# Kernel optimization log

Hardware: AMD Instinct MI355X
Metric: run time of the kernel (lower is better)

Reference implementation:

```python
import jax, jax.numpy as jnp
import numpy as np

B, N, DIM, H, DH, M = 4, 1024, 1024, 16, 64, 16  # batch, seq, model dim, heads, head dim, num_mem_kv
QK_SCALE = 10.0  # qk_norm_scale


def l2norm(t, eps=1e-12):
    # F.normalize(t, dim=-1) with clamp_min(eps), groups=1
    n = jnp.linalg.norm(t, axis=-1, keepdims=True)
    return t / jnp.maximum(n, eps)


def rotate_half(x):
    # interleaved pairs: (x0,x1) -> (-x1, x0)
    x = x.reshape(*x.shape[:-1], -1, 2)
    x1, x2 = x[..., 0], x[..., 1]
    return jnp.stack((-x2, x1), axis=-1).reshape(*x.shape[:-2], x.shape[-2] * 2)


def apply_rope(t, freqs):
    # freqs: [n, d], t: [b, h, n, d]
    return t * jnp.cos(freqs) + rotate_half(t) * jnp.sin(freqs)


def setup_inputs() -> dict:
    key = jax.random.key(0)
    ks = jax.random.split(key, 14)
    x = jax.random.normal(ks[0], (B, N, DIM), dtype=jnp.float32)
    # rotary freqs: outer(pos, inv_freq) with each freq repeated twice (interleaved pairs)
    pos = jnp.arange(N, dtype=jnp.float32)
    inv_freq = 1.0 / (10000.0 ** (jnp.arange(0, DH, 2, dtype=jnp.float32) / DH))
    freqs = jnp.repeat(pos[:, None] * inv_freq[None, :], 2, axis=-1)  # [N, DH]
    s = 0.02
    Wq = jax.random.normal(ks[1], (DIM, H * DH), dtype=jnp.float32) * s
    Wk = jax.random.normal(ks[2], (DIM, H * DH), dtype=jnp.float32) * s
    Wv = jax.random.normal(ks[3], (DIM, H * DH), dtype=jnp.float32) * s
    q_scale = 1.0 + 0.1 * jax.random.normal(ks[4], (H, 1, DH), dtype=jnp.float32)
    k_scale = 1.0 + 0.1 * jax.random.normal(ks[5], (H, 1, DH), dtype=jnp.float32)
    mem_k = jax.random.normal(ks[6], (H, M, DH), dtype=jnp.float32)
    mem_v = jax.random.normal(ks[7], (H, M, DH), dtype=jnp.float32)
    W_pre = jnp.eye(H, dtype=jnp.float32) + 0.05 * jax.random.normal(ks[8], (H, H), dtype=jnp.float32)
    W_post = jnp.eye(H, dtype=jnp.float32) + 0.05 * jax.random.normal(ks[9], (H, H), dtype=jnp.float32)
    W_hgate = jax.random.normal(ks[10], (DIM, H), dtype=jnp.float32) * s
    b_hgate = jnp.full((H,), 2.0, dtype=jnp.float32)
    W_vgate = jax.random.normal(ks[11], (DIM, H * DH), dtype=jnp.float32) * s
    b_vgate = jnp.full((H * DH,), 2.0, dtype=jnp.float32)
    Wo = jax.random.normal(ks[12], (H * DH, DIM), dtype=jnp.float32) * s
    return dict(x=x, freqs=freqs, Wq=Wq, Wk=Wk, Wv=Wv, q_scale=q_scale, k_scale=k_scale,
                mem_k=mem_k, mem_v=mem_v, W_pre=W_pre, W_post=W_post,
                W_hgate=W_hgate, b_hgate=b_hgate, W_vgate=W_vgate, b_vgate=b_vgate, Wo=Wo)


def reference(x, freqs, Wq, Wk, Wv, q_scale, k_scale, mem_k, mem_v,
              W_pre, W_post, W_hgate, b_hgate, W_vgate, b_vgate, Wo):
    b, n, _ = x.shape
    # projections -> [b, h, n, dh]
    q = (x @ Wq).reshape(b, n, H, DH).transpose(0, 2, 1, 3)
    k = (x @ Wk).reshape(b, n, H, DH).transpose(0, 2, 1, 3)
    v = (x @ Wv).reshape(b, n, H, DH).transpose(0, 2, 1, 3)
    # qk l2-norm (groups=1) + learned per-head dim scales
    q = l2norm(q) * q_scale
    k = l2norm(k) * k_scale
    # rotary (xpos_scale = None -> scale 1)
    q = apply_rope(q, freqs)
    k = apply_rope(k, freqs)
    # memory key/values, prepended along the kv sequence axis
    mk = (l2norm(mem_k) * k_scale)[None].repeat(b, axis=0)  # [b,h,M,dh]
    mv = mem_v[None].repeat(b, axis=0)
    k = jnp.concatenate((mk, k), axis=-2)  # [b,h,M+n,dh]
    v = jnp.concatenate((mv, v), axis=-2)
    i, j = q.shape[-2], k.shape[-2]
    dots = jnp.einsum('bhid,bhjd->bhij', q, k) * QK_SCALE
    dots = jnp.einsum('bhij,gh->bgij', dots, W_pre)  # pre-softmax talking heads
    # causal mask (memory slots at the front are always visible)
    qpos = jnp.arange(i)
    kpos = jnp.arange(j)
    causal = kpos[None, :] > (qpos[:, None] + (j - i))  # True -> masked
    mask_value = -jnp.finfo(dots.dtype).max
    dots = jnp.where(causal[None, None], mask_value, dots)
    attn = jax.nn.softmax(dots, axis=-1)
    attn = jnp.einsum('bhij,gh->bgij', attn, W_post)  # post-softmax talking heads
    out = jnp.einsum('bhij,bhjd->bhid', attn, v)  # [b,h,n,dh]
    # per-head value gate
    head_gate = jax.nn.sigmoid(x @ W_hgate + b_hgate)  # [b,n,h]
    out = out * head_gate.transpose(0, 2, 1)[..., None]
    out = out.transpose(0, 2, 1, 3).reshape(b, n, H * DH)
    # per-dim value gate (sigmoid)
    out = out * jax.nn.sigmoid(x @ W_vgate + b_vgate)
    return out @ Wo
```

## Files before the change

### kernel.cpp

```cpp
#include <hip/hip_runtime.h>
#include <hip/hip_bf16.h>
#include <cmath>

typedef __attribute__((ext_vector_type(8))) short short8;
typedef __attribute__((ext_vector_type(4))) float f32x4;

__device__ __forceinline__ unsigned short to_bf(float f) {
  __hip_bfloat16 h = __float2bfloat16(f);
  return __builtin_bit_cast(unsigned short, h);
}

#define SWZS(ir) ((((ir) & 1) << 4) | (((ir) & 6) << 1))

__global__ __launch_bounds__(256)
void cvt_bf16x4(const float* __restrict__ in, unsigned short* __restrict__ out, int n4)
{
  int i = blockIdx.x * 256 + threadIdx.x;
  if (i < n4) {
    float4 v = ((const float4*)in)[i];
    ushort4 o;
    o.x = to_bf(v.x); o.y = to_bf(v.y); o.z = to_bf(v.z); o.w = to_bf(v.w);
    ((ushort4*)out)[i] = o;
  }
}

__global__ __launch_bounds__(256)
void transpose_to_bf(const float* __restrict__ W, unsigned short* __restrict__ WT)
{
  __shared__ float tile[64][65];
  const int n0 = blockIdx.x * 64, k0 = blockIdx.y * 64;
  const int t = threadIdx.x, c = t & 63, r4 = t >> 6;
#pragma unroll
  for (int q = 0; q < 16; ++q) {
    int r = (q << 2) + r4;
    tile[r][c] = W[(size_t)(k0 + r) * 1024 + n0 + c];
  }
  __syncthreads();
#pragma unroll
  for (int q = 0; q < 16; ++q) {
    int r = (q << 2) + r4;
    WT[(size_t)(n0 + r) * 1024 + k0 + c] = to_bf(tile[c][r]);
  }
}

__global__ __launch_bounds__(256)
void transpose4_to_bf(const float* __restrict__ W0, const float* __restrict__ W1,
                      const float* __restrict__ W2, const float* __restrict__ W3,
                      unsigned short* __restrict__ WT4)
{
  __shared__ float tile[64][65];
  const float* W = (blockIdx.z == 0) ? W0 : (blockIdx.z == 1) ? W1
                 : (blockIdx.z == 2) ? W2 : W3;
  const int n0 = blockIdx.x * 64, k0 = blockIdx.y * 64;
  const int t = threadIdx.x, c = t & 63, r4 = t >> 6;
#pragma unroll
  for (int q = 0; q < 16; ++q) {
    int r = (q << 2) + r4;
    tile[r][c] = W[(size_t)(k0 + r) * 1024 + n0 + c];
  }
  __syncthreads();
  const size_t zoff = (size_t)blockIdx.z << 10;
#pragma unroll
  for (int q = 0; q < 16; ++q) {
    int r = (q << 2) + r4;
    WT4[(zoff + n0 + r) * 1024 + k0 + c] = to_bf(tile[c][r]);
  }
}

__global__ __launch_bounds__(256)
void gemm_bf128(const unsigned short* __restrict__ A, const unsigned short* __restrict__ BT,
                float* __restrict__ C)
{
  __shared__ __align__(16) unsigned short Ab[128 * 36];
  __shared__ __align__(16) unsigned short Bb[64 * 36];
  const int t = threadIdx.x, lane = t & 63, w = t >> 6;
  const int m = lane & 15, quad = lane >> 4;
  const int row0 = blockIdx.y << 7, col0 = blockIdx.x << 6;

  const int r0 = t >> 2, kp0 = t & 3;
  const int r1 = 64 + r0;

  f32x4 acc[2][4];
#pragma unroll
  for (int mi = 0; mi < 2; ++mi)
#pragma unroll
    for (int ni = 0; ni < 4; ++ni) acc[mi][ni] = (f32x4){0.f, 0.f, 0.f, 0.f};

  uint4 pa0 = *(const uint4*)(A + (size_t)(row0 + r0) * 1024 + kp0 * 8);
  uint4 pa1 = *(const uint4*)(A + (size_t)(row0 + r1) * 1024 + kp0 * 8);
  uint4 pb0 = *(const uint4*)(BT + (size_t)(col0 + r0) * 1024 + kp0 * 8);

  for (int kk = 0; kk < 1024; kk += 32) {
    *(uint4*)((char*)Ab + r0 * 72 + kp0 * 16) = pa0;
    *(uint4*)((char*)Ab + r1 * 72 + kp0 * 16) = pa1;
    *(uint4*)((char*)Bb + r0 * 72 + kp0 * 16) = pb0;
    __syncthreads();
    if (kk + 32 < 1024) {
      pa0 = *(const uint4*)(A + (size_t)(row0 + r0) * 1024 + kk + 32 + kp0 * 8);
      pa1 = *(const uint4*)(A + (size_t)(row0 + r1) * 1024 + kk + 32 + kp0 * 8);
      pb0 = *(const uint4*)(BT + (size_t)(col0 + r0) * 1024 + kk + 32 + kp0 * 8);
    }
    short8 af[2], bf[4];
#pragma unroll
    for (int mi = 0; mi < 2; ++mi)
      af[mi] = *(const short8*)((char*)Ab + ((w << 5) + (mi << 4) + m) * 72 + quad * 16);
#pragma unroll
    for (int ni = 0; ni < 4; ++ni)
      bf[ni] = *(const short8*)((char*)Bb + ((ni << 4) + m) * 72 + quad * 16);
#pragma unroll
    for (int mi = 0; mi < 2; ++mi)
#pragma unroll
      for (int ni = 0; ni < 4; ++ni)
        acc[mi][ni] = __builtin_amdgcn_mfma_f32_16x16x32_bf16(af[mi], bf[ni], acc[mi][ni], 0, 0, 0);
    __syncthreads();
  }
#pragma unroll
  for (int mi = 0; mi < 2; ++mi)
#pragma unroll
    for (int ni = 0; ni < 4; ++ni)
#pragma unroll
      for (int reg = 0; reg < 4; ++reg) {
        int mrow = row0 + (w << 5) + (mi << 4) + (quad << 2) + reg;
        int ncol = col0 + (ni << 4) + m;
        C[((size_t)mrow << 10) + ncol] = acc[mi][ni][reg];
      }
}

__global__ __launch_bounds__(256)
void gemm_qkvg(const unsigned short* __restrict__ A, const unsigned short* __restrict__ BT4,
               float* __restrict__ q_lin, float* __restrict__ k_lin,
               unsigned short* __restrict__ vallT, float* __restrict__ vgbuf,
               const float* __restrict__ b_vg)
{
  __shared__ __align__(16) unsigned short Ab[128 * 36];
  __shared__ __align__(16) unsigned short Bb[64 * 36];
  const int t = threadIdx.x, lane = t & 63, w = t >> 6;
  const int m = lane & 15, quad = lane >> 4;
  const int row0 = blockIdx.y << 7, col0 = blockIdx.x << 6;
  const int sector = col0 >> 10;

  const int r0 = t >> 2, kp0 = t & 3;
  const int r1 = 64 + r0;

  f32x4 acc[2][4];
#pragma unroll
  for (int mi = 0; mi < 2; ++mi)
#pragma unroll
    for (int ni = 0; ni < 4; ++ni) acc[mi][ni] = (f32x4){0.f, 0.f, 0.f, 0.f};

  uint4 pa0 = *(const uint4*)(A + (size_t)(row0 + r0) * 1024 + kp0 * 8);
  uint4 pa1 = *(const uint4*)(A + (size_t)(row0 + r1) * 1024 + kp0 * 8);
  uint4 pb0 = *(const uint4*)(BT4 + (size_t)(col0 + r0) * 1024 + kp0 * 8);

  for (int kk = 0; kk < 1024; kk += 32) {
    *(uint4*)((char*)Ab + r0 * 72 + kp0 * 16) = pa0;
    *(uint4*)((char*)Ab + r1 * 72 + kp0 * 16) = pa1;
    *(uint4*)((char*)Bb + r0 * 72 + kp0 * 16) = pb0;
    __syncthreads();
    if (kk + 32 < 1024) {
      pa0 = *(const uint4*)(A + (size_t)(row0 + r0) * 1024 + kk + 32 + kp0 * 8);
      pa1 = *(const uint4*)(A + (size_t)(row0 + r1) * 1024 + kk + 32 + kp0 * 8);
      pb0 = *(const uint4*)(BT4 + (size_t)(col0 + r0) * 1024 + kk + 32 + kp0 * 8);
    }
    short8 af[2], bf[4];
#pragma unroll
    for (int mi = 0; mi < 2; ++mi)
      af[mi] = *(const short8*)((char*)Ab + ((w << 5) + (mi << 4) + m) * 72 + quad * 16);
#pragma unroll
    for (int ni = 0; ni < 4; ++ni)
      bf[ni] = *(const short8*)((char*)Bb + ((ni << 4) + m) * 72 + quad * 16);
#pragma unroll
    for (int mi = 0; mi < 2; ++mi)
#pragma unroll
      for (int ni = 0; ni < 4; ++ni)
        acc[mi][ni] = __builtin_amdgcn_mfma_f32_16x16x32_bf16(af[mi], bf[ni], acc[mi][ni], 0, 0, 0);
    __syncthreads();
  }
#pragma unroll
  for (int mi = 0; mi < 2; ++mi)
#pragma unroll
    for (int ni = 0; ni < 4; ++ni)
#pragma unroll
      for (int reg = 0; reg < 4; ++reg) {
        int mrow = row0 + (w << 5) + (mi << 4) + (quad << 2) + reg;
        int nl = (col0 & 1023) + (ni << 4) + m;
        float v = acc[mi][ni][reg];
        if (sector == 0) {
          q_lin[((size_t)mrow << 10) + nl] = v;
        } else if (sector == 1) {
          k_lin[((size_t)mrow << 10) + nl] = v;
        } else if (sector == 2) {
          int bb = mrow >> 10, nn = mrow & 1023;
          vallT[((size_t)((bb << 10) + nl)) * 1056 + 16 + nn] = to_bf(v);
        } else {
          float s = v + b_vg[nl];
          vgbuf[((size_t)mrow << 10) + nl] = 1.f / (1.f + __expf(-s));
        }
      }
}

__global__ __launch_bounds__(256)
void hgate_proj(const float* __restrict__ x, const float* __restrict__ W,
                const float* __restrict__ bias, float* __restrict__ hg)
{
  int G = blockIdx.x * 256 + threadIdx.x;
  int row = G >> 4, h = G & 15;
  const float4* x4 = (const float4*)(x + ((size_t)row << 10));
  float acc = 0.f;
#pragma unroll 4
  for (int k4 = 0; k4 < 256; ++k4) {
    float4 xv = x4[k4];
    int kb = k4 << 2;
    acc += xv.x * W[(kb + 0) * 16 + h] + xv.y * W[(kb + 1) * 16 + h]
         + xv.z * W[(kb + 2) * 16 + h] + xv.w * W[(kb + 3) * 16 + h];
  }
  float v = acc + bias[h];
  hg[(row << 4) + h] = 1.f / (1.f + __expf(-v));
}

__global__ __launch_bounds__(256)
void q_post_bf(const float* __restrict__ q_lin, const float* __restrict__ scale,
               const float* __restrict__ freqs, unsigned short* __restrict__ qb)
{
  int gid = blockIdx.x * 256 + threadIdx.x;
  int d = gid & 63;
  int row = gid >> 6;
  int h = row & 15;
  int n = (row >> 4) & 1023;
  float v = q_lin[gid];
  float ss = v * v;
#pragma unroll
  for (int off = 32; off; off >>= 1) ss += __shfl_xor(ss, off);
  v = v / fmaxf(sqrtf(ss), 1e-12f) * scale[(h << 6) + d];
  float f = freqs[(n << 6) + d];
  float other = __shfl_xor(v, 1);
  float rot = (d & 1) ? other : -other;
  qb[gid] = to_bf((v * cosf(f) + rot * sinf(f)) * 10.f);
}

__global__ __launch_bounds__(256)
void k_post_bf(const float* __restrict__ k_lin, const float* __restrict__ scale,
               const float* __restrict__ freqs, unsigned short* __restrict__ kall)
{
  int gid = blockIdx.x * 256 + threadIdx.x;
  int d = gid & 63;
  int row = gid >> 6;
  int h = row & 15;
  int n = (row >> 4) & 1023;
  int b = row >> 14;
  float v = k_lin[gid];
  float ss = v * v;
#pragma unroll
  for (int off = 32; off; off >>= 1) ss += __shfl_xor(ss, off);
  v = v / fmaxf(sqrtf(ss), 1e-12f) * scale[(h << 6) + d];
  float f = freqs[(n << 6) + d];
  float other = __shfl_xor(v, 1);
  float rot = (d & 1) ? other : -other;
  float out = v * cosf(f) + rot * sinf(f);
  kall[(size_t)(b * 1056 + 16 + n) * 1024 + (h << 6) + d] = to_bf(out);
}

__global__ __launch_bounds__(256)
void mem_build(const float* __restrict__ mem_k, const float* __restrict__ mem_v,
               const float* __restrict__ k_scale,
               unsigned short* __restrict__ kall, unsigned short* __restrict__ vallT)
{
  int gid = blockIdx.x * 256 + threadIdx.x;
  int d = gid & 63;
  int row = gid >> 6;
  int h = row >> 4, mm = row & 15;
  float v = mem_k[gid];
  float ss = v * v;
#pragma unroll
  for (int off = 32; off; off >>= 1) ss += __shfl_xor(ss, off);
  unsigned short kb = to_bf(v / fmaxf(sqrtf(ss), 1e-12f) * k_scale[(h << 6) + d]);
  unsigned short vb = to_bf(mem_v[gid]);
#pragma unroll
  for (int b = 0; b < 4; ++b) {
    kall[(size_t)(b * 1056 + mm) * 1024 + (h << 6) + d] = kb;
    vallT[(size_t)((b << 10) + (h << 6) + d) * 1056 + mm] = vb;
  }
}


__global__ __launch_bounds__(256)
void attn_lsum(const unsigned short* __restrict__ qb, const unsigned short* __restrict__ kall,
               const float* __restrict__ W_pre, float* __restrict__ Lbuf)
{
  __shared__ float sS[16 * 16 * 32];
  __shared__ f32x4 sWpre4[64];

  const int t = threadIdx.x, lane = t & 63, w = t >> 6;
  const int m = lane & 15, quad = lane >> 4;
  if (t < 64) {
    int h = t >> 2, p4 = t & 3;
    sWpre4[t] = (f32x4){W_pre[(4 * p4 + 0) * 16 + h], W_pre[(4 * p4 + 1) * 16 + h],
                        W_pre[(4 * p4 + 2) * 16 + h], W_pre[(4 * p4 + 3) * 16 + h]};
  }

  const int blk = blockIdx.x;
  const int u0 = (4352 * blk) / 768, u1 = (4352 * (blk + 1)) / 768;
  if (u0 == u1) return;

  int accu = 0, bi = 0;
  while (true) {
    int un = (((bi & 63) + 1) >> 1) + 1;
    if (accu + un > u0) break;
    accu += un; ++bi;
  }
  int b = bi >> 6, it = bi & 63, uoff = u0 - accu;

  short8 afr[4][2];
  float partL[16];
  bool fresh = true;

  for (int u = u0; u < u1; ++u) {
    const int i0 = it << 4;
    if (fresh) {
#pragma unroll
      for (int hh = 0; hh < 4; ++hh)
#pragma unroll
        for (int kk = 0; kk < 2; ++kk)
          afr[hh][kk] = *(const short8*)(qb + (((size_t)(b << 10) + i0 + m) << 10)
                                         + ((w << 2) + hh) * 64 + kk * 32 + quad * 8);
#pragma unroll
      for (int g = 0; g < 16; ++g) partL[g] = 0.f;
      fresh = false;
    }
    const int j0 = uoff << 5;
#pragma unroll
    for (int sub = 0; sub < 2; ++sub) {
      const int js = j0 + (sub << 4);
#pragma unroll
      for (int hh = 0; hh < 4; ++hh) {
        f32x4 s = (f32x4){0.f, 0.f, 0.f, 0.f};
#pragma unroll
        for (int kk = 0; kk < 2; ++kk) {
          short8 bfr = *(const short8*)(kall + ((size_t)(b * 1056 + js + m) << 10)
                                        + ((w << 2) + hh) * 64 + kk * 32 + quad * 8);
          s = __builtin_amdgcn_mfma_f32_16x16x32_bf16(afr[hh][kk], bfr, s, 0, 0, 0);
        }
#pragma unroll
        for (int reg = 0; reg < 4; ++reg) {
          int irow = (quad << 2) + reg;
          sS[(((w << 2) + hh) * 16 + irow) * 32 + (((sub << 4) + m) ^ SWZS(irow))] = s[reg];
        }
      }
    }
    __syncthreads();
    {
      const int i_l = t >> 4, j_l = t & 15;
      const int ig = i0 + i_l;
      const int vs = SWZS(i_l);
      const int sc0 = j_l ^ vs, sc1 = (16 + j_l) ^ vs;
      float ch0[16], ch1[16];
#pragma unroll
      for (int h = 0; h < 16; ++h) {
        ch0[h] = sS[(h * 16 + i_l) * 32 + sc0];
        ch1[h] = sS[(h * 16 + i_l) * 32 + sc1];
      }
      f32x4 a0[4], a1[4];
#pragma unroll
      for (int p = 0; p < 4; ++p) { a0[p] = (f32x4){0.f,0.f,0.f,0.f}; a1[p] = a0[p]; }
#pragma unroll
      for (int h = 0; h < 16; ++h) {
        float c0 = ch0[h], c1 = ch1[h];
#pragma unroll
        for (int p = 0; p < 4; ++p) {
          f32x4 wv = sWpre4[(h << 2) + p];
          a0[p] += wv * c0;
          a1[p] += wv * c1;
        }
      }
      const bool ok0 = (j0 + j_l) <= ig + 16;
      const bool ok1 = (j0 + 16 + j_l) <= ig + 16;
#pragma unroll
      for (int p = 0; p < 4; ++p)
#pragma unroll
        for (int e = 0; e < 4; ++e) {
          float v0 = ok0 ? __expf(a0[p][e] - 20.f) : 0.f;
          float v1 = ok1 ? __expf(a1[p][e] - 20.f) : 0.f;
          partL[(p << 2) + e] += v0 + v1;
        }
    }
    __syncthreads();
    ++uoff;
    if (uoff == ((it + 1) >> 1) + 1) {
#pragma unroll
      for (int g = 0; g < 16; ++g) {
        float v = partL[g];
        v += __shfl_xor(v, 1); v += __shfl_xor(v, 2);
        v += __shfl_xor(v, 4); v += __shfl_xor(v, 8);
        if (m == 0)
          atomicAdd(&Lbuf[(((size_t)(b << 10) + i0 + (w << 2) + quad) << 4) + g], v);
      }
      ++bi; b = bi >> 6; it = bi & 63; uoff = 0; fresh = true;
    }
  }
  if (!fresh) {
    const int i0 = it << 4;
#pragma unroll
    for (int g = 0; g < 16; ++g) {
      float v = partL[g];
      v += __shfl_xor(v, 1); v += __shfl_xor(v, 2);
      v += __shfl_xor(v, 4); v += __shfl_xor(v, 8);
      if (m == 0)
        atomicAdd(&Lbuf[(((size_t)(b << 10) + i0 + (w << 2) + quad) << 4) + g], v);
    }
  }
}

__global__ __launch_bounds__(256)
void attn_pv2(const unsigned short* __restrict__ qb, const unsigned short* __restrict__ kall,
              const unsigned short* __restrict__ vallT, const float* __restrict__ W_pre,
              const float* __restrict__ W_post, const float* __restrict__ Lbuf,
              float* __restrict__ Obuf)
{
  __shared__ float sS[16 * 16 * 32];
  __shared__ __align__(16) unsigned short sE[16 * 16 * 32];
  __shared__ f32x4 sWpre4[64], sWpost4[64];
  __shared__ float sIL[256];

  const int t = threadIdx.x, lane = t & 63, w = t >> 6;
  const int m = lane & 15, quad = lane >> 4;
  if (t < 64) {
    int h = t >> 2, p4 = t & 3;
    sWpre4[t]  = (f32x4){W_pre[(4 * p4 + 0) * 16 + h],  W_pre[(4 * p4 + 1) * 16 + h],
                         W_pre[(4 * p4 + 2) * 16 + h],  W_pre[(4 * p4 + 3) * 16 + h]};
    sWpost4[t] = (f32x4){W_post[(4 * p4 + 0) * 16 + h], W_post[(4 * p4 + 1) * 16 + h],
                         W_post[(4 * p4 + 2) * 16 + h], W_post[(4 * p4 + 3) * 16 + h]};
  }

  const int blk = blockIdx.x;
  const int u0 = (4352 * blk) / 768, u1 = (4352 * (blk + 1)) / 768;
  if (u0 == u1) return;

  int accu = 0, bi = 0;
  while (true) {
    int un = (((bi & 63) + 1) >> 1) + 1;
    if (accu + un > u0) break;
    accu += un; ++bi;
  }
  int b = bi >> 6, it = bi & 63, uoff = u0 - accu;

  short8 afr[4][2];
  f32x4 oacc[4][4];
  bool fresh = true;

  for (int u = u0; u < u1; ++u) {
    const int i0 = it << 4;
    if (fresh) {
#pragma unroll
      for (int hh = 0; hh < 4; ++hh)
#pragma unroll
        for (int kk = 0; kk < 2; ++kk)
          afr[hh][kk] = *(const short8*)(qb + (((size_t)(b << 10) + i0 + m) << 10)
                                         + ((w << 2) + hh) * 64 + kk * 32 + quad * 8);
#pragma unroll
      for (int a = 0; a < 4; ++a)
#pragma unroll
        for (int dt = 0; dt < 4; ++dt) oacc[a][dt] = (f32x4){0.f, 0.f, 0.f, 0.f};
      sIL[t] = 1.f / Lbuf[(((size_t)(b << 10) + i0 + (t >> 4)) << 4) + (t & 15)];
      fresh = false;
    }
    const int j0 = uoff << 5;
#pragma unroll
    for (int sub = 0; sub < 2; ++sub) {
      const int js = j0 + (sub << 4);
#pragma unroll
      for (int hh = 0; hh < 4; ++hh) {
        f32x4 s = (f32x4){0.f, 0.f, 0.f, 0.f};
#pragma unroll
        for (int kk = 0; kk < 2; ++kk) {
          short8 bfr = *(const short8*)(kall + ((size_t)(b * 1056 + js + m) << 10)
                                        + ((w << 2) + hh) * 64 + kk * 32 + quad * 8);
          s = __builtin_amdgcn_mfma_f32_16x16x32_bf16(afr[hh][kk], bfr, s, 0, 0, 0);
        }
#pragma unroll
        for (int reg = 0; reg < 4; ++reg) {
          int irow = (quad << 2) + reg;
          sS[(((w << 2) + hh) * 16 + irow) * 32 + (((sub << 4) + m) ^ SWZS(irow))] = s[reg];
        }
      }
    }
    __syncthreads();
    {
      const int i_l = t >> 4, j_l = t & 15;
      const int ig = i0 + i_l;
      const int vs = SWZS(i_l);
      const int sc0 = j_l ^ vs, sc1 = (16 + j_l) ^ vs;
      const int r3s = i_l & 3;
      const int eo0 = ((((j_l >> 3) ^ r3s) << 3) | (j_l & 7));
      const int eo1 = ((((2 + (j_l >> 3)) ^ r3s) << 3) | (j_l & 7));
      float ch0[16], ch1[16];
#pragma unroll
      for (int h = 0; h < 16; ++h) {
        ch0[h] = sS[(h * 16 + i_l) * 32 + sc0];
        ch1[h] = sS[(h * 16 + i_l) * 32 + sc1];
      }
      f32x4 a0[4], a1[4];
#pragma unroll
      for (int p = 0; p < 4; ++p) { a0[p] = (f32x4){0.f,0.f,0.f,0.f}; a1[p] = a0[p]; }
#pragma unroll
      for (int h = 0; h < 16; ++h) {
        float c0 = ch0[h], c1 = ch1[h];
#pragma unroll
        for (int p = 0; p < 4; ++p) {
          f32x4 wv = sWpre4[(h << 2) + p];
          a0[p] += wv * c0;
          a1[p] += wv * c1;
        }
      }
      const bool ok0 = (j0 + j_l) <= ig + 16;
      const bool ok1 = (j0 + 16 + j_l) <= ig + 16;
      float e0[16], e1[16];
#pragma unroll
      for (int p = 0; p < 4; ++p)
#pragma unroll
        for (int e = 0; e < 4; ++e) {
          int g = (p << 2) + e;
          float il = sIL[(i_l << 4) + g];
          e0[g] = ok0 ? __expf(a0[p][e] - 20.f) * il : 0.f;
          e1[g] = ok1 ? __expf(a1[p][e] - 20.f) * il : 0.f;
        }
      f32x4 b0[4], b1[4];
#pragma unroll
      for (int p = 0; p < 4; ++p) { b0[p] = (f32x4){0.f,0.f,0.f,0.f}; b1[p] = b0[p]; }
#pragma unroll
      for (int g = 0; g < 16; ++g) {
        float c0 = e0[g], c1 = e1[g];
#pragma unroll
        for (int p = 0; p < 4; ++p) {
          f32x4 wv = sWpost4[(g << 2) + p];
          b0[p] += wv * c0;
          b1[p] += wv * c1;
        }
      }
#pragma unroll
      for (int p = 0; p < 4; ++p)
#pragma unroll
        for (int e = 0; e < 4; ++e) {
          int g2 = (p << 2) + e;
          sE[(g2 * 16 + i_l) * 32 + eo0] = to_bf(b0[p][e]);
          sE[(g2 * 16 + i_l) * 32 + eo1] = to_bf(b1[p][e]);
        }
    }
    __syncthreads();
#pragma unroll
    for (int gl = 0; gl < 4; ++gl) {
      const int g2 = (w << 2) + gl;
      short8 a = *(const short8*)(sE + (g2 * 16 + m) * 32 + ((quad ^ (m & 3)) << 3));
#pragma unroll
      for (int dt = 0; dt < 4; ++dt) {
        short8 bv = *(const short8*)(vallT + ((size_t)((b << 10) + g2 * 64 + dt * 16 + m)) * 1056
                                     + j0 + quad * 8);
        oacc[gl][dt] = __builtin_amdgcn_mfma_f32_16x16x32_bf16(a, bv, oacc[gl][dt], 0, 0, 0);
      }
    }
    ++uoff;
    if (uoff == ((it + 1) >> 1) + 1) {
#pragma unroll
      for (int gl = 0; gl < 4; ++gl) {
        int g2 = (w << 2) + gl;
#pragma unroll
        for (int dt = 0; dt < 4; ++dt)
#pragma unroll
          for (int reg = 0; reg < 4; ++reg)
            atomicAdd(&Obuf[(((size_t)(b << 10) + i0 + (quad << 2) + reg) << 10)
                            + g2 * 64 + dt * 16 + m], oacc[gl][dt][reg]);
      }
      ++bi; b = bi >> 6; it = bi & 63; uoff = 0; fresh = true;
    }
  }
  if (!fresh) {
    const int i0 = it << 4;
#pragma unroll
    for (int gl = 0; gl < 4; ++gl) {
      int g2 = (w << 2) + gl;
#pragma unroll
      for (int dt = 0; dt < 4; ++dt)
#pragma unroll
        for (int reg = 0; reg < 4; ++reg)
          atomicAdd(&Obuf[(((size_t)(b << 10) + i0 + (quad << 2) + reg) << 10)
                          + g2 * 64 + dt * 16 + m], oacc[gl][dt][reg]);
    }
  }
}

__global__ __launch_bounds__(256)
void gate_out(const float* __restrict__ Obuf, const float* __restrict__ hgate,
              const float* __restrict__ vgate, unsigned short* __restrict__ aob)
{
  int i4 = blockIdx.x * 256 + threadIdx.x;
  float4 o = ((const float4*)Obuf)[i4];
  int base = i4 << 2;
  int row = base >> 10, hd = base & 1023, h = hd >> 6;
  float hg = hgate[(row << 4) + h];
  float4 vg = ((const float4*)vgate)[i4];
  ushort4 r;
  r.x = to_bf(o.x * hg * vg.x);
  r.y = to_bf(o.y * hg * vg.y);
  r.z = to_bf(o.z * hg * vg.z);
  r.w = to_bf(o.w * hg * vg.w);
  ((ushort4*)aob)[i4] = r;
}

extern "C" void kernel_launch(void* const* d_in, const int* in_sizes, int n_in,
                              void* d_out, int out_size, void* d_ws, size_t ws_size,
                              hipStream_t stream)
{
  const float* x       = (const float*)d_in[0];
  const float* freqs   = (const float*)d_in[1];
  const float* Wq      = (const float*)d_in[2];
  const float* Wk      = (const float*)d_in[3];
  const float* Wv      = (const float*)d_in[4];
  const float* q_scale = (const float*)d_in[5];
  const float* k_scale = (const float*)d_in[6];
  const float* mem_k   = (const float*)d_in[7];
  const float* mem_v   = (const float*)d_in[8];
  const float* W_pre   = (const float*)d_in[9];
  const float* W_post  = (const float*)d_in[10];
  const float* W_hg    = (const float*)d_in[11];
  const float* b_hg    = (const float*)d_in[12];
  const float* W_vg    = (const float*)d_in[13];
  const float* b_vg    = (const float*)d_in[14];
  const float* Wo      = (const float*)d_in[15];
  float* out = (float*)d_out;
  float* ws  = (float*)d_ws;

  float* q_lin = ws;
  unsigned short* aob = (unsigned short*)ws;
  float* Lbuf  = ws + 4128768;
  float* k_lin = ws + 4194304;
  float* Obuf  = k_lin;
  float* vgbuf = ws + 8388608;
  float* hgbuf = ws + 12582912;
  unsigned short* xb   = (unsigned short*)(ws + 12713984);
  unsigned short* qb   = xb;
  unsigned short* kall = (unsigned short*)(ws + 14811136);
  unsigned short* vallT= (unsigned short*)(ws + 16973824);
  unsigned short* wb4  = kall;

  dim3 blk(256);
  cvt_bf16x4<<<4096, blk, 0, stream>>>(x, xb, 1048576);
  hgate_proj<<<256, blk, 0, stream>>>(x, W_hg, b_hg, hgbuf);
  transpose4_to_bf<<<dim3(16, 16, 4), blk, 0, stream>>>(Wq, Wk, Wv, W_vg, wb4);
  gemm_qkvg<<<dim3(64, 32), blk, 0, stream>>>(xb, wb4, q_lin, k_lin, vallT, vgbuf, b_vg);
  q_post_bf<<<16384, blk, 0, stream>>>(q_lin, q_scale, freqs, qb);
  k_post_bf<<<16384, blk, 0, stream>>>(k_lin, k_scale, freqs, kall);
  mem_build<<<64, blk, 0, stream>>>(mem_k, mem_v, k_scale, kall, vallT);
  hipMemsetAsync(Lbuf, 0, (65536 + 4194304) * sizeof(float), stream);
  attn_lsum<<<768, blk, 0, stream>>>(qb, kall, W_pre, Lbuf);
  attn_pv2<<<768, blk, 0, stream>>>(qb, kall, vallT, W_pre, W_post, Lbuf, Obuf);
  gate_out<<<4096, blk, 0, stream>>>(Obuf, hgbuf, vgbuf, aob);
  transpose_to_bf<<<dim3(16, 16), blk, 0, stream>>>(Wo, wb4);
  gemm_bf128<<<dim3(16, 32), blk, 0, stream>>>(aob, wb4, out);
}
```

Baseline: 507.6 us.

## Use direct global-to-LDS loads with double-buffered tiles in projection GEMMs

Both bf16 GEMM kernels now stage A and B tiles straight from global memory into LDS with global_load_lds instead of going through registers, and alternate between two LDS buffers so the next tile loads while the current one feeds MFMA. This is meant to hide load latency and remove register staging and one barrier per iteration. The padded 72-byte row stride becomes an unpadded 64-byte stride, which may add LDS bank conflicts on the fragment reads. It also relies on the implicit per-wave contiguous LDS layout matching the row/k mapping.

```diff
diff --git a/kernel.cpp b/kernel.cpp
--- a/kernel.cpp
+++ b/kernel.cpp
@@ -8,6 +8,11 @@
 __device__ __forceinline__ unsigned short to_bf(float f) {
   __hip_bfloat16 h = __float2bfloat16(f);
   return __builtin_bit_cast(unsigned short, h);
+}
+
+__device__ __forceinline__ void gload_lds16(const void* g, void* l) {
+  __builtin_amdgcn_global_load_lds((const __attribute__((address_space(1))) void*)g,
+                                   (__attribute__((address_space(3))) void*)l, 16, 0, 0);
 }
 
 #define SWZS(ir) ((((ir) & 1) << 4) | (((ir) & 6) << 1))
@@ -71,14 +76,13 @@
 void gemm_bf128(const unsigned short* __restrict__ A, const unsigned short* __restrict__ BT,
                 float* __restrict__ C)
 {
-  __shared__ __align__(16) unsigned short Ab[128 * 36];
-  __shared__ __align__(16) unsigned short Bb[64 * 36];
+  __shared__ __align__(16) unsigned short Ab[2][128 * 32];
+  __shared__ __align__(16) unsigned short Bb[2][64 * 32];
   const int t = threadIdx.x, lane = t & 63, w = t >> 6;
   const int m = lane & 15, quad = lane >> 4;
   const int row0 = blockIdx.y << 7, col0 = blockIdx.x << 6;
 
   const int r0 = t >> 2, kp0 = t & 3;
-  const int r1 = 64 + r0;
 
   f32x4 acc[2][4];
 #pragma unroll
@@ -86,33 +90,36 @@
 #pragma unroll
     for (int ni = 0; ni < 4; ++ni) acc[mi][ni] = (f32x4){0.f, 0.f, 0.f, 0.f};
 
-  uint4 pa0 = *(const uint4*)(A + (size_t)(row0 + r0) * 1024 + kp0 * 8);
-  uint4 pa1 = *(const uint4*)(A + (size_t)(row0 + r1) * 1024 + kp0 * 8);
-  uint4 pb0 = *(const uint4*)(BT + (size_t)(col0 + r0) * 1024 + kp0 * 8);
-
+  const unsigned short* gA0 = A + (size_t)(row0 + r0) * 1024 + kp0 * 8;
+  const unsigned short* gA1 = A + (size_t)(row0 + 64 + r0) * 1024 + kp0 * 8;
+  const unsigned short* gB0 = BT + (size_t)(col0 + r0) * 1024 + kp0 * 8;
+  const int wb = w << 10;
+
+#define STAGE_WO(buf, kk) do {                                            \
+    gload_lds16(gA0 + (kk), (char*)&Ab[buf][0] + wb);                     \
+    gload_lds16(gA1 + (kk), (char*)&Ab[buf][0] + 4096 + wb);              \
+    gload_lds16(gB0 + (kk), (char*)&Bb[buf][0] + wb);                     \
+  } while (0)
+
+  STAGE_WO(0, 0);
+  __syncthreads();
+  int cur = 0;
   for (int kk = 0; kk < 1024; kk += 32) {
-    *(uint4*)((char*)Ab + r0 * 72 + kp0 * 16) = pa0;
-    *(uint4*)((char*)Ab + r1 * 72 + kp0 * 16) = pa1;
-    *(uint4*)((char*)Bb + r0 * 72 + kp0 * 16) = pb0;
-    __syncthreads();
-    if (kk + 32 < 1024) {
-      pa0 = *(const uint4*)(A + (size_t)(row0 + r0) * 1024 + kk + 32 + kp0 * 8);
-      pa1 = *(const uint4*)(A + (size_t)(row0 + r1) * 1024 + kk + 32 + kp0 * 8);
-      pb0 = *(const uint4*)(BT + (size_t)(col0 + r0) * 1024 + kk + 32 + kp0 * 8);
-    }
+    if (kk + 32 < 1024) STAGE_WO(cur ^ 1, kk + 32);
     short8 af[2], bf[4];
 #pragma unroll
     for (int mi = 0; mi < 2; ++mi)
-      af[mi] = *(const short8*)((char*)Ab + ((w << 5) + (mi << 4) + m) * 72 + quad * 16);
+      af[mi] = *(const short8*)((char*)&Ab[cur][0] + ((w << 5) + (mi << 4) + m) * 64 + quad * 16);
 #pragma unroll
     for (int ni = 0; ni < 4; ++ni)
-      bf[ni] = *(const short8*)((char*)Bb + ((ni << 4) + m) * 72 + quad * 16);
+      bf[ni] = *(const short8*)((char*)&Bb[cur][0] + ((ni << 4) + m) * 64 + quad * 16);
 #pragma unroll
     for (int mi = 0; mi < 2; ++mi)
 #pragma unroll
       for (int ni = 0; ni < 4; ++ni)
         acc[mi][ni] = __builtin_amdgcn_mfma_f32_16x16x32_bf16(af[mi], bf[ni], acc[mi][ni], 0, 0, 0);
     __syncthreads();
+    cur ^= 1;
   }
 #pragma unroll
   for (int mi = 0; mi < 2; ++mi)
@@ -132,15 +139,14 @@
                unsigned short* __restrict__ vallT, float* __restrict__ vgbuf,
                const float* __restrict__ b_vg)
 {
-  __shared__ __align__(16) unsigned short Ab[128 * 36];
-  __shared__ __align__(16) unsigned short Bb[64 * 36];
+  __shared__ __align__(16) unsigned short Ab[2][128 * 32];
+  __shared__ __align__(16) unsigned short Bb[2][64 * 32];
   const int t = threadIdx.x, lane = t & 63, w = t >> 6;
   const int m = lane & 15, quad = lane >> 4;
   const int row0 = blockIdx.y << 7, col0 = blockIdx.x << 6;
   const int sector = col0 >> 10;
 
   const int r0 = t >> 2, kp0 = t & 3;
-  const int r1 = 64 + r0;
 
   f32x4 acc[2][4];
 #pragma unroll
@@ -148,33 +154,36 @@
 #pragma unroll
     for (int ni = 0; ni < 4; ++ni) acc[mi][ni] = (f32x4){0.f, 0.f, 0.f, 0.f};
 
-  uint4 pa0 = *(const uint4*)(A + (size_t)(row0 + r0) * 1024 + kp0 * 8);
-  uint4 pa1 = *(const uint4*)(A + (size_t)(row0 + r1) * 1024 + kp0 * 8);
-  uint4 pb0 = *(const uint4*)(BT4 + (size_t)(col0 + r0) * 1024 + kp0 * 8);
-
+  const unsigned short* gA0 = A + (size_t)(row0 + r0) * 1024 + kp0 * 8;
+  const unsigned short* gA1 = A + (size_t)(row0 + 64 + r0) * 1024 + kp0 * 8;
+  const unsigned short* gB0 = BT4 + (size_t)(col0 + r0) * 1024 + kp0 * 8;
+  const int wb = w << 10;
+
+#define STAGE_QK(buf, kk) do {                                            \
+    gload_lds16(gA0 + (kk), (char*)&Ab[buf][0] + wb);                     \
+    gload_lds16(gA1 + (kk), (char*)&Ab[buf][0] + 4096 + wb);              \
+    gload_lds16(gB0 + (kk), (char*)&Bb[buf][0] + wb);                     \
+  } while (0)
+
+  STAGE_QK(0, 0);
+  __syncthreads();
+  int cur = 0;
   for (int kk = 0; kk < 1024; kk += 32) {
-    *(uint4*)((char*)Ab + r0 * 72 + kp0 * 16) = pa0;
-    *(uint4*)((char*)Ab + r1 * 72 + kp0 * 16) = pa1;
-    *(uint4*)((char*)Bb + r0 * 72 + kp0 * 16) = pb0;
-    __syncthreads();
-    if (kk + 32 < 1024) {
-      pa0 = *(const uint4*)(A + (size_t)(row0 + r0) * 1024 + kk + 32 + kp0 * 8);
-      pa1 = *(const uint4*)(A + (size_t)(row0 + r1) * 1024 + kk + 32 + kp0 * 8);
-      pb0 = *(const uint4*)(BT4 + (size_t)(col0 + r0) * 1024 + kk + 32 + kp0 * 8);
-    }
+    if (kk + 32 < 1024) STAGE_QK(cur ^ 1, kk + 32);
     short8 af[2], bf[4];
 #pragma unroll
     for (int mi = 0; mi < 2; ++mi)
-      af[mi] = *(const short8*)((char*)Ab + ((w << 5) + (mi << 4) + m) * 72 + quad * 16);
+      af[mi] = *(const short8*)((char*)&Ab[cur][0] + ((w << 5) + (mi << 4) + m) * 64 + quad * 16);
 #pragma unroll
     for (int ni = 0; ni < 4; ++ni)
-      bf[ni] = *(const short8*)((char*)Bb + ((ni << 4) + m) * 72 + quad * 16);
+      bf[ni] = *(const short8*)((char*)&Bb[cur][0] + ((ni << 4) + m) * 64 + quad * 16);
 #pragma unroll
     for (int mi = 0; mi < 2; ++mi)
 #pragma unroll
       for (int ni = 0; ni < 4; ++ni)
         acc[mi][ni] = __builtin_amdgcn_mfma_f32_16x16x32_bf16(af[mi], bf[ni], acc[mi][ni], 0, 0, 0);
     __syncthreads();
+    cur ^= 1;
   }
 #pragma unroll
   for (int mi = 0; mi < 2; ++mi)
```

Result: no change. 514.8 us (+1.4%).
